# Performance work log

Hardware: AMD Instinct MI355X
Metric: run time of the kernel (lower is better)

## Reference

```python
import jax, jax.numpy as jnp
import numpy as np

B, S, D, H = 2, 2048, 1024, 16
DH = D // H


def setup_inputs() -> dict:
    key = jax.random.key(0)
    ks = jax.random.split(key, 5)
    scale = 1.0 / np.sqrt(D)
    return {
        "x": jax.random.normal(ks[0], (B, S, D), dtype=jnp.float32),
        "Wq": jax.random.normal(ks[1], (D, D), dtype=jnp.float32) * scale,
        "bq": jnp.zeros((D,), jnp.float32),
        "Wk": jax.random.normal(ks[2], (D, D), dtype=jnp.float32) * scale,
        "bk": jnp.zeros((D,), jnp.float32),
        "Wv": jax.random.normal(ks[3], (D, D), dtype=jnp.float32) * scale,
        "bv": jnp.zeros((D,), jnp.float32),
        "Wo": jax.random.normal(ks[4], (D, D), dtype=jnp.float32) * scale,
        "bo": jnp.zeros((D,), jnp.float32),
    }


def reference(x, Wq, bq, Wk, bk, Wv, bv, Wo, bo):
    b, s, d = x.shape
    # QKV projections (torch Linear: x @ W.T + b)
    q = (x @ Wq.T + bq).reshape(b, s, H, DH).transpose(0, 2, 1, 3)  # [b,h,s,dh]
    k = (x @ Wk.T + bk).reshape(b, s, H, DH).transpose(0, 2, 1, 3)
    v = (x @ Wv.T + bv).reshape(b, s, H, DH).transpose(0, 2, 1, 3)
    scale = 1.0 / jnp.sqrt(jnp.array(DH, dtype=jnp.float32))
    energy = jnp.einsum("bhqd,bhkd->bhqk", q, k) * scale  # [b,h,s,s]
    attn = jax.nn.softmax(energy, axis=-1)
    out = jnp.einsum("bhqk,bhkd->bhqd", attn, v)  # [b,h,s,dh]
    out = out.transpose(0, 2, 1, 3).reshape(b, s, d)
    return out @ Wo.T + bo
```

## Files before the change

### kernel.cpp

```cpp
#include <hip/hip_runtime.h>

using bf16x8 = __attribute__((ext_vector_type(8))) short;
using f32x4  = __attribute__((ext_vector_type(4))) float;
using u32x2  = __attribute__((ext_vector_type(2))) unsigned int;

__device__ __forceinline__ unsigned short f2bf(float f) {
  union { float f; unsigned int u; } v; v.f = f;
  unsigned int u = v.u;
  unsigned int r = (u + 0x7FFFu + ((u >> 16) & 1u)) >> 16;
  return (unsigned short)r;
}

__device__ __forceinline__ unsigned int pk2bf(float a, float b) {
  union { float f; unsigned int u; } x, y; x.f = a; y.f = b;
  unsigned int ua = x.u + 0x7FFFu + ((x.u >> 16) & 1u);
  unsigned int ub = y.u + 0x7FFFu + ((y.u >> 16) & 1u);
  return __builtin_amdgcn_perm(ub, ua, 0x07060302u);
}

__device__ __forceinline__ void gl_lds16(const void* g, void* l) {
  __builtin_amdgcn_global_load_lds(
      (const __attribute__((address_space(1))) void*)g,
      (__attribute__((address_space(3))) void*)l, 16, 0, 0);
}

__global__ void cast_all(const float* __restrict__ x,
                         const float* __restrict__ wq, const float* __restrict__ wk,
                         const float* __restrict__ wv, const float* __restrict__ wo,
                         unsigned short* __restrict__ xb,
                         unsigned short* __restrict__ wqb, unsigned short* __restrict__ wkb,
                         unsigned short* __restrict__ wvb, unsigned short* __restrict__ wob) {
  size_t i4 = ((size_t)blockIdx.x * 256 + threadIdx.x) * 4;
  const float* src; unsigned short* dst; size_t off;
  if (i4 < 4194304) { src = x; dst = xb; off = i4; }
  else {
    size_t j = i4 - 4194304;
    int w = (int)(j >> 20);
    off = j & 1048575;
    src = (w == 0) ? wq : (w == 1) ? wk : (w == 2) ? wv : wo;
    dst = (w == 0) ? wqb : (w == 1) ? wkb : (w == 2) ? wvb : wob;
  }
  float4 v = *(const float4*)(src + off);
  ushort4 o;
  o.x = f2bf(v.x); o.y = f2bf(v.y); o.z = f2bf(v.z); o.w = f2bf(v.w);
  *(ushort4*)(dst + off) = o;
}

template <int BN>
__device__ __forceinline__ void gemm_tile_nt(const unsigned short* __restrict__ A,
                                             const unsigned short* __restrict__ Bm,
                                             int tile_m, int tile_n,
                                             f32x4 acc[4][BN / 32]) {
  constexpr int JN = BN / 32;
  __shared__ __align__(16) unsigned short As[128 * 32];
  __shared__ __align__(16) unsigned short Bs[BN * 32];
  const int tid = threadIdx.x;
  const int lane = tid & 63, wave = tid >> 6;
  const int quad = lane >> 4, l16 = lane & 15;
  const int wm = (wave & 1) * 64, wn = (wave >> 1) * (BN / 2);
  const int srow = tid >> 2;
  const int scol = (tid & 3) * 8;

#pragma unroll
  for (int i = 0; i < 4; i++)
#pragma unroll
    for (int j = 0; j < JN; j++)
#pragma unroll
      for (int r = 0; r < 4; r++) acc[i][j][r] = 0.f;

  for (int k0 = 0; k0 < 1024; k0 += 32) {
#pragma unroll
    for (int t = 0; t < 2; t++)
      gl_lds16(A + (size_t)(tile_m + t * 64 + srow) * 1024 + k0 + scol,
               (char*)As + t * 4096 + tid * 16);
    if (BN == 128) {
#pragma unroll
      for (int t = 0; t < 2; t++)
        gl_lds16(Bm + (size_t)(tile_n + t * 64 + srow) * 1024 + k0 + scol,
                 (char*)Bs + t * 4096 + tid * 16);
    } else {
      gl_lds16(Bm + (size_t)(tile_n + srow) * 1024 + k0 + scol, (char*)Bs + tid * 16);
    }
    __syncthreads();
    bf16x8 a[4], b[JN];
#pragma unroll
    for (int i = 0; i < 4; i++)
      a[i] = *(const bf16x8*)((const char*)As + ((wm + i * 16 + l16) * 32 + quad * 8) * 2);
#pragma unroll
    for (int j = 0; j < JN; j++)
      b[j] = *(const bf16x8*)((const char*)Bs + ((wn + j * 16 + l16) * 32 + quad * 8) * 2);
#pragma unroll
    for (int i = 0; i < 4; i++)
#pragma unroll
      for (int j = 0; j < JN; j++)
        acc[i][j] = __builtin_amdgcn_mfma_f32_16x16x32_bf16(a[i], b[j], acc[i][j], 0, 0, 0);
    __syncthreads();
  }
}

__global__ __launch_bounds__(256) void gemm_qkv(
    const unsigned short* __restrict__ xb,
    const unsigned short* __restrict__ wqb, const unsigned short* __restrict__ wkb,
    const unsigned short* __restrict__ wvb,
    const float* __restrict__ bq, const float* __restrict__ bk, const float* __restrict__ bv,
    unsigned short* __restrict__ Qo, unsigned short* __restrict__ Ko,
    unsigned short* __restrict__ Vt) {
  const int z = blockIdx.z;
  const unsigned short* Bm = (z == 0) ? wqb : (z == 1) ? wkb : wvb;
  const float* bias = (z == 0) ? bq : (z == 1) ? bk : bv;
  const int tile_m = blockIdx.y * 128, tile_n = blockIdx.x * 128;
  f32x4 acc[4][4];
  gemm_tile_nt<128>(xb, Bm, tile_m, tile_n, acc);

  const int tid = threadIdx.x, lane = tid & 63, wave = tid >> 6;
  const int quad = lane >> 4, l16 = lane & 15;
  const int wm = (wave & 1) * 64, wn = (wave >> 1) * 64;
  const float scale = (z == 0) ? 0.125f : 1.0f;

  if (z < 2) {
    unsigned short* out = (z == 0) ? Qo : Ko;
#pragma unroll
    for (int i = 0; i < 4; i++)
#pragma unroll
      for (int j = 0; j < 4; j++) {
        int n = tile_n + wn + j * 16 + l16;
        float bn = bias[n];
#pragma unroll
        for (int r = 0; r < 4; r++) {
          int m = tile_m + wm + i * 16 + quad * 4 + r;
          out[(size_t)m * 1024 + n] = f2bf((acc[i][j][r] + bn) * scale);
        }
      }
  } else {
#pragma unroll
    for (int i = 0; i < 4; i++)
#pragma unroll
      for (int j = 0; j < 4; j++) {
        int n = tile_n + wn + j * 16 + l16;
        int hh = n >> 6, dh = n & 63;
        float bn = bias[n];
        int m0 = tile_m + wm + i * 16 + quad * 4;
        int b = m0 >> 11, s = m0 & 2047;
        ushort4 pk;
        pk.x = f2bf(acc[i][j][0] + bn);
        pk.y = f2bf(acc[i][j][1] + bn);
        pk.z = f2bf(acc[i][j][2] + bn);
        pk.w = f2bf(acc[i][j][3] + bn);
        *(ushort4*)(Vt + ((size_t)((b * 16 + hh) * 64 + dh)) * 2048 + s) = pk;
      }
  }
}

__global__ __launch_bounds__(256, 2) void flash_attn(
    const unsigned short* __restrict__ Qg, const unsigned short* __restrict__ Kg,
    const unsigned short* __restrict__ Vt, unsigned short* __restrict__ AO) {
  __shared__ __align__(16) unsigned short Kl[8 * 128 * 8];
  __shared__ __align__(16) unsigned short Vl[16 * 64 * 8];
  __shared__ __align__(16) unsigned short Pl[4 * 32 * 136];

  const int tid = threadIdx.x, lane = tid & 63, wave = tid >> 6;
  const int quad = lane >> 4, l16 = lane & 15;
  const int bi = blockIdx.x;
  const int bh = (bi & 7) * 4 + ((bi >> 3) & 3);
  const int qt = bi >> 5;
  const int b = bh >> 4, h = bh & 15;
  unsigned short* Pw = Pl + wave * (32 * 136);

  const size_t qbase = ((size_t)(b * 2048 + qt * 128 + wave * 32)) * 1024 + h * 64;
  bf16x8 qf[2][2];
#pragma unroll
  for (int qs = 0; qs < 2; qs++)
#pragma unroll
    for (int ks = 0; ks < 2; ks++)
      qf[qs][ks] = *(const bf16x8*)(Qg + qbase + (size_t)(qs * 16 + l16) * 1024 +
                                    ks * 32 + quad * 8);

  f32x4 O[2][4];
  float lp[2] = {0.f, 0.f};
#pragma unroll
  for (int qs = 0; qs < 2; qs++)
#pragma unroll
    for (int mb = 0; mb < 4; mb++)
#pragma unroll
      for (int r = 0; r < 4; r++) O[qs][mb][r] = 0.f;

  for (int kt = 0; kt < 16; kt++) {
    __syncthreads();
    const size_t krow0 = (size_t)(b * 2048 + kt * 128);
#pragma unroll
    for (int t = 0; t < 4; t++) {
      int i = t * 256 + tid; int g = i >> 7, row = i & 127;
      gl_lds16(Kg + (krow0 + row) * 1024 + h * 64 + g * 8, (char*)Kl + i * 16);
    }
    const size_t vbase = ((size_t)bh * 64) * 2048 + (size_t)kt * 128;
#pragma unroll
    for (int t = 0; t < 4; t++) {
      int i = t * 256 + tid; int g = i >> 6, d = i & 63;
      gl_lds16(Vt + vbase + (size_t)d * 2048 + g * 8, (char*)Vl + i * 16);
    }
    __syncthreads();

    f32x4 sacc[2][8];
#pragma unroll
    for (int qs = 0; qs < 2; qs++)
#pragma unroll
      for (int nb = 0; nb < 8; nb++)
#pragma unroll
        for (int r = 0; r < 4; r++) sacc[qs][nb][r] = 0.f;
#pragma unroll
    for (int nb = 0; nb < 8; nb++) {
      bf16x8 kf0 = *(const bf16x8*)((const char*)Kl + ((quad) * 128 + nb * 16 + l16) * 16);
      bf16x8 kf1 = *(const bf16x8*)((const char*)Kl + ((4 + quad) * 128 + nb * 16 + l16) * 16);
#pragma unroll
      for (int qs = 0; qs < 2; qs++) {
        sacc[qs][nb] = __builtin_amdgcn_mfma_f32_16x16x32_bf16(kf0, qf[qs][0], sacc[qs][nb], 0, 0, 0);
        sacc[qs][nb] = __builtin_amdgcn_mfma_f32_16x16x32_bf16(kf1, qf[qs][1], sacc[qs][nb], 0, 0, 0);
      }
    }

#pragma unroll
    for (int qs = 0; qs < 2; qs++) {
#pragma unroll
      for (int nb = 0; nb < 8; nb++) {
        float p0 = __expf(sacc[qs][nb][0]);
        float p1 = __expf(sacc[qs][nb][1]);
        float p2 = __expf(sacc[qs][nb][2]);
        float p3 = __expf(sacc[qs][nb][3]);
        lp[qs] += (p0 + p1) + (p2 + p3);
        u32x2 d; d[0] = pk2bf(p0, p1); d[1] = pk2bf(p2, p3);
        *(u32x2*)(Pw + (qs * 16 + l16) * 136 + nb * 16 + quad * 4) = d;
      }
    }

#pragma unroll
    for (int kc = 0; kc < 4; kc++) {
      bf16x8 pf[2];
#pragma unroll
      for (int qs = 0; qs < 2; qs++)
        pf[qs] = *(const bf16x8*)(Pw + (qs * 16 + l16) * 136 + kc * 32 + quad * 8);
#pragma unroll
      for (int mb = 0; mb < 4; mb++) {
        bf16x8 vf = *(const bf16x8*)((const char*)Vl + ((kc * 4 + quad) * 64 + mb * 16 + l16) * 16);
#pragma unroll
        for (int qs = 0; qs < 2; qs++)
          O[qs][mb] = __builtin_amdgcn_mfma_f32_16x16x32_bf16(vf, pf[qs], O[qs][mb], 0, 0, 0);
      }
    }
  }

  float inv[2];
#pragma unroll
  for (int qs = 0; qs < 2; qs++) {
    float l = lp[qs];
    l += __shfl_xor(l, 16);
    l += __shfl_xor(l, 32);
    inv[qs] = 1.f / l;
  }

#pragma unroll
  for (int qs = 0; qs < 2; qs++)
#pragma unroll
    for (int mb = 0; mb < 4; mb++) {
      float o0 = O[qs][mb][0] * inv[qs];
      float o1 = O[qs][mb][1] * inv[qs];
      float o2 = O[qs][mb][2] * inv[qs];
      float o3 = O[qs][mb][3] * inv[qs];
      u32x2 d; d[0] = pk2bf(o0, o1); d[1] = pk2bf(o2, o3);
      *(u32x2*)(Pw + (qs * 16 + l16) * 72 + mb * 16 + quad * 4) = d;
    }
  const size_t orow0 = (size_t)(b * 2048 + qt * 128 + wave * 32);
#pragma unroll
  for (int p = 0; p < 4; p++) {
    int q = p * 8 + (lane >> 3), dh = (lane & 7) * 8;
    bf16x8 o = *(const bf16x8*)(Pw + q * 72 + dh);
    *(bf16x8*)(AO + (orow0 + q) * 1024 + h * 64 + dh) = o;
  }
}

__global__ __launch_bounds__(256) void gemm_out(
    const unsigned short* __restrict__ AO, const unsigned short* __restrict__ wob,
    const float* __restrict__ bo, float* __restrict__ out) {
  const int tile_m = blockIdx.y * 128, tile_n = blockIdx.x * 64;
  f32x4 acc[4][2];
  gemm_tile_nt<64>(AO, wob, tile_m, tile_n, acc);
  const int tid = threadIdx.x, lane = tid & 63, wave = tid >> 6;
  const int quad = lane >> 4, l16 = lane & 15;
  const int wm = (wave & 1) * 64, wn = (wave >> 1) * 32;
#pragma unroll
  for (int i = 0; i < 4; i++)
#pragma unroll
    for (int j = 0; j < 2; j++) {
      int n = tile_n + wn + j * 16 + l16;
      float bn = bo[n];
#pragma unroll
      for (int r = 0; r < 4; r++) {
        int m = tile_m + wm + i * 16 + quad * 4 + r;
        out[(size_t)m * 1024 + n] = acc[i][j][r] + bn;
      }
    }
}

extern "C" void kernel_launch(void* const* d_in, const int* in_sizes, int n_in,
                              void* d_out, int out_size, void* d_ws, size_t ws_size,
                              hipStream_t stream) {
  (void)in_sizes; (void)n_in; (void)out_size; (void)ws_size;
  const float* x  = (const float*)d_in[0];
  const float* Wq = (const float*)d_in[1];
  const float* bq = (const float*)d_in[2];
  const float* Wk = (const float*)d_in[3];
  const float* bk = (const float*)d_in[4];
  const float* Wv = (const float*)d_in[5];
  const float* bv = (const float*)d_in[6];
  const float* Wo = (const float*)d_in[7];
  const float* bo = (const float*)d_in[8];
  float* out = (float*)d_out;

  char* ws = (char*)d_ws;
  unsigned short* xb  = (unsigned short*)(ws + 0);
  unsigned short* wqb = (unsigned short*)(ws + 8388608);
  unsigned short* wkb = (unsigned short*)(ws + 10485760);
  unsigned short* wvb = (unsigned short*)(ws + 12582912);
  unsigned short* wob = (unsigned short*)(ws + 14680064);
  unsigned short* Qb  = (unsigned short*)(ws + 16777216);
  unsigned short* Kb  = (unsigned short*)(ws + 25165824);
  unsigned short* Vtb = (unsigned short*)(ws + 33554432);
  unsigned short* AOb = (unsigned short*)(ws + 41943040);

  cast_all<<<8192, 256, 0, stream>>>(x, Wq, Wk, Wv, Wo, xb, wqb, wkb, wvb, wob);
  gemm_qkv<<<dim3(8, 32, 3), dim3(256), 0, stream>>>(xb, wqb, wkb, wvb, bq, bk, bv, Qb, Kb, Vtb);
  flash_attn<<<512, 256, 0, stream>>>(Qb, Kb, Vtb, AOb);
  gemm_out<<<dim3(16, 32, 1), dim3(256), 0, stream>>>(AOb, wob, bo, out);
}
```

Measured before the change: 223.8 us.

## Double-buffer K/V tiles in flash attention and shrink the P staging buffer

K and V tiles now go into two LDS buffers. The next tile's async global-to-LDS load is issued right after the loop-top barrier, so it overlaps the current tile's QK^T, softmax and PV work, and one of the two barriers per iteration is dropped. The probability tile is kept packed in registers and written to a small per-wave 32-column LDS chunk just before each PV step, instead of a full 128-column staging array. The output staging reuses the K/V buffer. In exchange, LDS use per block grows and register pressure rises from holding the packed P values, which could hurt occupancy at two blocks per CU.

```diff
diff --git a/kernel.cpp b/kernel.cpp
--- a/kernel.cpp
+++ b/kernel.cpp
@@ -154,9 +154,8 @@
 __global__ __launch_bounds__(256, 2) void flash_attn(
     const unsigned short* __restrict__ Qg, const unsigned short* __restrict__ Kg,
     const unsigned short* __restrict__ Vt, unsigned short* __restrict__ AO) {
-  __shared__ __align__(16) unsigned short Kl[8 * 128 * 8];
-  __shared__ __align__(16) unsigned short Vl[16 * 64 * 8];
-  __shared__ __align__(16) unsigned short Pl[4 * 32 * 136];
+  __shared__ __align__(16) unsigned short KV[2][16384];
+  __shared__ __align__(16) unsigned short Pc[4][32][40];
 
   const int tid = threadIdx.x, lane = tid & 63, wave = tid >> 6;
   const int quad = lane >> 4, l16 = lane & 15;
@@ -164,7 +163,6 @@
   const int bh = (bi & 7) * 4 + ((bi >> 3) & 3);
   const int qt = bi >> 5;
   const int b = bh >> 4, h = bh & 15;
-  unsigned short* Pw = Pl + wave * (32 * 136);
 
   const size_t qbase = ((size_t)(b * 2048 + qt * 128 + wave * 32)) * 1024 + h * 64;
   bf16x8 qf[2][2];
@@ -184,21 +182,33 @@
 #pragma unroll
       for (int r = 0; r < 4; r++) O[qs][mb][r] = 0.f;
 
+  const size_t kbase = (size_t)(b * 2048) * 1024 + h * 64;
+  const size_t vbase = (size_t)(bh * 64) * 2048;
+
+  auto stage = [&](int kt) {
+    char* Kl = (char*)&KV[kt & 1][0];
+    char* Vl = (char*)&KV[kt & 1][8192];
+#pragma unroll
+    for (int t = 0; t < 4; t++) {
+      int i = t * 256 + tid; int g = i >> 7, row = i & 127;
+      gl_lds16(Kg + kbase + (size_t)(kt * 128 + row) * 1024 + g * 8, Kl + i * 16);
+    }
+#pragma unroll
+    for (int t = 0; t < 4; t++) {
+      int i = t * 256 + tid; int g = i >> 6, d = i & 63;
+      gl_lds16(Vt + vbase + (size_t)d * 2048 + kt * 128 + g * 8, Vl + i * 16);
+    }
+  };
+
+  stage(0);
+
   for (int kt = 0; kt < 16; kt++) {
     __syncthreads();
-    const size_t krow0 = (size_t)(b * 2048 + kt * 128);
-#pragma unroll
-    for (int t = 0; t < 4; t++) {
-      int i = t * 256 + tid; int g = i >> 7, row = i & 127;
-      gl_lds16(Kg + (krow0 + row) * 1024 + h * 64 + g * 8, (char*)Kl + i * 16);
-    }
-    const size_t vbase = ((size_t)bh * 64) * 2048 + (size_t)kt * 128;
-#pragma unroll
-    for (int t = 0; t < 4; t++) {
-      int i = t * 256 + tid; int g = i >> 6, d = i & 63;
-      gl_lds16(Vt + vbase + (size_t)d * 2048 + g * 8, (char*)Vl + i * 16);
-    }
-    __syncthreads();
+    if (kt < 15) stage(kt + 1);
+    __builtin_amdgcn_sched_barrier(0);
+
+    const char* Kl = (const char*)&KV[kt & 1][0];
+    const char* Vl = (const char*)&KV[kt & 1][8192];
 
     f32x4 sacc[2][8];
 #pragma unroll
@@ -209,8 +219,8 @@
         for (int r = 0; r < 4; r++) sacc[qs][nb][r] = 0.f;
 #pragma unroll
     for (int nb = 0; nb < 8; nb++) {
-      bf16x8 kf0 = *(const bf16x8*)((const char*)Kl + ((quad) * 128 + nb * 16 + l16) * 16);
-      bf16x8 kf1 = *(const bf16x8*)((const char*)Kl + ((4 + quad) * 128 + nb * 16 + l16) * 16);
+      bf16x8 kf0 = *(const bf16x8*)(Kl + ((quad) * 128 + nb * 16 + l16) * 16);
+      bf16x8 kf1 = *(const bf16x8*)(Kl + ((4 + quad) * 128 + nb * 16 + l16) * 16);
 #pragma unroll
       for (int qs = 0; qs < 2; qs++) {
         sacc[qs][nb] = __builtin_amdgcn_mfma_f32_16x16x32_bf16(kf0, qf[qs][0], sacc[qs][nb], 0, 0, 0);
@@ -218,8 +228,9 @@
       }
     }
 
-#pragma unroll
-    for (int qs = 0; qs < 2; qs++) {
+    unsigned int pk[2][8][2];
+#pragma unroll
+    for (int qs = 0; qs < 2; qs++)
 #pragma unroll
       for (int nb = 0; nb < 8; nb++) {
         float p0 = __expf(sacc[qs][nb][0]);
@@ -227,20 +238,26 @@
         float p2 = __expf(sacc[qs][nb][2]);
         float p3 = __expf(sacc[qs][nb][3]);
         lp[qs] += (p0 + p1) + (p2 + p3);
-        u32x2 d; d[0] = pk2bf(p0, p1); d[1] = pk2bf(p2, p3);
-        *(u32x2*)(Pw + (qs * 16 + l16) * 136 + nb * 16 + quad * 4) = d;
-      }
-    }
+        pk[qs][nb][0] = pk2bf(p0, p1);
+        pk[qs][nb][1] = pk2bf(p2, p3);
+      }
 
 #pragma unroll
     for (int kc = 0; kc < 4; kc++) {
+#pragma unroll
+      for (int qs = 0; qs < 2; qs++)
+#pragma unroll
+        for (int t = 0; t < 2; t++) {
+          u32x2 d; d[0] = pk[qs][2 * kc + t][0]; d[1] = pk[qs][2 * kc + t][1];
+          *(u32x2*)(&Pc[wave][qs * 16 + l16][t * 16 + quad * 4]) = d;
+        }
       bf16x8 pf[2];
 #pragma unroll
       for (int qs = 0; qs < 2; qs++)
-        pf[qs] = *(const bf16x8*)(Pw + (qs * 16 + l16) * 136 + kc * 32 + quad * 8);
+        pf[qs] = *(const bf16x8*)(&Pc[wave][qs * 16 + l16][quad * 8]);
 #pragma unroll
       for (int mb = 0; mb < 4; mb++) {
-        bf16x8 vf = *(const bf16x8*)((const char*)Vl + ((kc * 4 + quad) * 64 + mb * 16 + l16) * 16);
+        bf16x8 vf = *(const bf16x8*)(Vl + ((kc * 4 + quad) * 64 + mb * 16 + l16) * 16);
 #pragma unroll
         for (int qs = 0; qs < 2; qs++)
           O[qs][mb] = __builtin_amdgcn_mfma_f32_16x16x32_bf16(vf, pf[qs], O[qs][mb], 0, 0, 0);
@@ -257,15 +274,14 @@
     inv[qs] = 1.f / l;
   }
 
+  unsigned short* Pw = (unsigned short*)&KV[0][0] + wave * (32 * 72);
 #pragma unroll
   for (int qs = 0; qs < 2; qs++)
 #pragma unroll
     for (int mb = 0; mb < 4; mb++) {
-      float o0 = O[qs][mb][0] * inv[qs];
-      float o1 = O[qs][mb][1] * inv[qs];
-      float o2 = O[qs][mb][2] * inv[qs];
-      float o3 = O[qs][mb][3] * inv[qs];
-      u32x2 d; d[0] = pk2bf(o0, o1); d[1] = pk2bf(o2, o3);
+      u32x2 d;
+      d[0] = pk2bf(O[qs][mb][0] * inv[qs], O[qs][mb][1] * inv[qs]);
+      d[1] = pk2bf(O[qs][mb][2] * inv[qs], O[qs][mb][3] * inv[qs]);
       *(u32x2*)(Pw + (qs * 16 + l16) * 72 + mb * 16 + quad * 4) = d;
     }
   const size_t orow0 = (size_t)(b * 2048 + qt * 128 + wave * 32);
```

Result: no change. 219.7 us (-1.9%).
